# Kernel optimization log

Measured on AMD Instinct MI355X. Metric: run time of the kernel, lower is better.

The kernel has to match this reference:

```python
import jax, jax.numpy as jnp
import numpy as np

E = 1024
H = 16
F = 4096
EPS = 1e-5


def layer_norm(x, gamma, beta):
    mu = jnp.mean(x, axis=-1, keepdims=True)
    var = jnp.var(x, axis=-1, keepdims=True)
    return (x - mu) * jax.lax.rsqrt(var + EPS) * gamma + beta


def setup_inputs() -> dict:
    key = jax.random.key(0)
    ks = jax.random.split(key, 12)
    s = lambda d: 1.0 / np.sqrt(d)
    x = jax.random.normal(ks[0], (2, 2048, E), dtype=jnp.float32)
    Wq = jax.random.uniform(ks[1], (E, E), minval=-s(E), maxval=s(E))
    bq = jnp.zeros((E,), jnp.float32)
    Wk = jax.random.uniform(ks[2], (E, E), minval=-s(E), maxval=s(E))
    bk = jnp.zeros((E,), jnp.float32)
    Wv = jax.random.uniform(ks[3], (E, E), minval=-s(E), maxval=s(E))
    bv = jnp.zeros((E,), jnp.float32)
    Wo = jax.random.uniform(ks[4], (E, E), minval=-s(E), maxval=s(E))
    bo = jnp.zeros((E,), jnp.float32)
    g1 = jnp.ones((E,), jnp.float32)
    b1 = jnp.zeros((E,), jnp.float32)
    W1 = jax.random.uniform(ks[5], (E, F), minval=-s(E), maxval=s(E))
    bf1 = jnp.zeros((F,), jnp.float32)
    W2 = jax.random.uniform(ks[6], (F, E), minval=-s(F), maxval=s(F))
    bf2 = jnp.zeros((E,), jnp.float32)
    g2 = jnp.ones((E,), jnp.float32)
    b2 = jnp.zeros((E,), jnp.float32)
    return dict(x=x, Wq=Wq, bq=bq, Wk=Wk, bk=bk, Wv=Wv, bv=bv, Wo=Wo, bo=bo,
                g1=g1, b1=b1, W1=W1, bf1=bf1, W2=W2, bf2=bf2, g2=g2, b2=b2)


def reference(x, Wq, bq, Wk, bk, Wv, bv, Wo, bo, g1, b1, W1, bf1, W2, bf2, g2, b2):
    B, L, _ = x.shape
    Dh = E // H
    q = (x @ Wq + bq).reshape(B, L, H, Dh).transpose(0, 2, 1, 3)  # b h l d
    k = (x @ Wk + bk).reshape(B, L, H, Dh).transpose(0, 2, 1, 3)  # computed but unused (faithful to source)
    v = (x @ Wv + bv).reshape(B, L, H, Dh).transpose(0, 2, 1, 3)
    # NOTE: source computes scores as Q @ V^T (not K), scaled, then softmax
    scores = jnp.einsum('bhqd,bhkd->bhqk', q, v) / jnp.sqrt(jnp.float32(Dh))
    att = jax.nn.softmax(scores, axis=-1)
    ctx = jnp.einsum('bhqk,bhkd->bhqd', att, v)
    ctx = ctx.transpose(0, 2, 1, 3).reshape(B, L, E)
    att_out = ctx @ Wo + bo
    post_att = layer_norm(x + att_out, g1, b1)
    ff = jax.nn.relu(post_att @ W1 + bf1) @ W2 + bf2
    return layer_norm(post_att + ff, g2, b2)
```

## Files before the change

### kernel.cpp

```cpp
#include <hip/hip_runtime.h>
#include <stdint.h>

typedef unsigned short u16;
typedef __attribute__((ext_vector_type(8))) short short8;
typedef __attribute__((ext_vector_type(4))) float f32x4;
typedef __attribute__((ext_vector_type(4))) unsigned short u16x4;

#define TOKENS 4096
#define E_DIM 1024
#define F_DIM 4096
#define SEQ 2048
#define NH 16
#define DH 64

__device__ __forceinline__ u16 f2b(float f) {
  union { float f; unsigned u; } v; v.f = f;
  unsigned r = v.u + 0x7fffu + ((v.u >> 16) & 1u);
  return (u16)(r >> 16);
}

__device__ __forceinline__ void gl2lds16(const u16* g, u16* l) {
  __builtin_amdgcn_global_load_lds(
      (const __attribute__((address_space(1))) unsigned int*)(size_t)(g),
      (__attribute__((address_space(3))) unsigned int*)(unsigned int)(size_t)(l),
      16, 0, 0);
}


__global__ __launch_bounds__(256)
void transpose_w(const float* __restrict__ W, u16* __restrict__ Wt, int K, int N) {
  __shared__ float tile[32][33];
  const int kb = blockIdx.x * 32, nb = blockIdx.y * 32;
  const int tx = threadIdx.x & 31, ty = threadIdx.x >> 5;
#pragma unroll
  for (int i = 0; i < 32; i += 8)
    tile[ty + i][tx] = W[(size_t)(kb + ty + i) * N + nb + tx];
  __syncthreads();
#pragma unroll
  for (int i = 0; i < 32; i += 8)
    Wt[(size_t)(nb + ty + i) * K + kb + tx] = f2b(tile[tx][ty + i]);
}

__global__ __launch_bounds__(256)
void f32_to_bf16(const float* __restrict__ in, u16* __restrict__ out) {
  const int i = blockIdx.x * 256 + threadIdx.x;
  f32x4 f = ((const f32x4*)in)[i];
  u16x4 u;
#pragma unroll
  for (int j = 0; j < 4; j++) u[j] = f2b(f[j]);
  ((u16x4*)out)[i] = u;
}

__global__ __launch_bounds__(256)
void transpose_v(const u16* __restrict__ vsrc, u16* __restrict__ vt) {
  __shared__ u16 tile[64][66];
  const int kb = blockIdx.x * 64;
  const int bh = blockIdx.y;
  const int b = bh >> 4, h = bh & 15;
  {
    const int d = threadIdx.x & 63, r = threadIdx.x >> 6;
#pragma unroll
    for (int i = 0; i < 64; i += 4)
      tile[r + i][d] = vsrc[(size_t)(b * SEQ + kb + r + i) * E_DIM + h * DH + d];
  }
  __syncthreads();
  {
    const int pos = threadIdx.x & 63;
    const int srck = (pos & 3) * 16 + (pos >> 2);
#pragma unroll
    for (int j = 0; j < 64; j += 4) {
      const int d = (threadIdx.x >> 6) + j;
      vt[(size_t)(bh * DH + d) * SEQ + kb + pos] = tile[srck][d];
    }
  }
}

template <int RELU, int OUTBF>
__global__ __launch_bounds__(512)
void gemm256(const u16* __restrict__ A, const u16* __restrict__ Bt,
             const float* __restrict__ bias, void* __restrict__ Cout,
             int N, int K) {
  __shared__ __align__(16) u16 lds[3][2][8192];
  const int tid = threadIdx.x;
  const int lane = tid & 63, wave = tid >> 6;
  const int wm = wave >> 2, wn = wave & 3;
  const int l15 = lane & 15, g = lane >> 4;

  const int bid = blockIdx.x;
  const int xcd = bid & 7, idx = bid >> 3;
  const int mT = (xcd >> 2) * 8 + (idx >> 2);
  const int nT = (xcd & 3) * 4 + (idx & 3);
  const int mBlk = mT * 256, nBlk = nT * 256;

  const u16* Ab = A + (size_t)mBlk * K;
  const u16* Bb = Bt + (size_t)nBlk * K;

  const int srow = lane >> 2;
  const int scolx = ((lane & 3) ^ ((lane >> 3) & 3)) * 8;
  const u16* sa0 = Ab + (size_t)(wave * 16 + srow) * K + scolx;
  const u16* sa1 = Ab + (size_t)((8 + wave) * 16 + srow) * K + scolx;
  const u16* sb0 = Bb + (size_t)(wave * 16 + srow) * K + scolx;
  const u16* sb1 = Bb + (size_t)((8 + wave) * 16 + srow) * K + scolx;

  const int fo = l15 * 32 + ((g ^ ((l15 >> 1) & 3)) << 3);

  f32x4 acc[8][4] = {};

  const int NT = K >> 5;

#define STAGE_A(buf, t)                                             \
  {                                                                 \
    gl2lds16(sa0 + (size_t)(t) * 32, &lds[buf][0][wave * 512 + lane * 8]);       \
    gl2lds16(sa1 + (size_t)(t) * 32, &lds[buf][0][(8 + wave) * 512 + lane * 8]); \
  }
#define STAGE_B(buf, t)                                             \
  {                                                                 \
    gl2lds16(sb0 + (size_t)(t) * 32, &lds[buf][1][wave * 512 + lane * 8]);       \
    gl2lds16(sb1 + (size_t)(t) * 32, &lds[buf][1][(8 + wave) * 512 + lane * 8]); \
  }

  STAGE_A(0, 0) STAGE_B(0, 0)
  STAGE_A(1, 1) STAGE_B(1, 1)
  asm volatile("s_waitcnt vmcnt(4)" ::: "memory");
  asm volatile("s_barrier" ::: "memory");

  int buf = 0, sbuf = 2;
  for (int t = 0; t < NT; ++t) {
    const u16* As_ = &lds[buf][0][wm * (8 * 512)];
    const u16* Bs_ = &lds[buf][1][wn * (4 * 512)];

    short8 af[4], bfr[4];
#pragma unroll
    for (int i = 0; i < 4; i++)
      af[i] = *(const short8*)(As_ + i * 512 + fo);
#pragma unroll
    for (int i = 0; i < 4; i++)
      bfr[i] = *(const short8*)(Bs_ + i * 512 + fo);
    if (t + 2 < NT) STAGE_A(sbuf, t + 2)
    asm volatile("s_barrier" ::: "memory");
    asm volatile("s_waitcnt lgkmcnt(0)" ::: "memory");
    __builtin_amdgcn_sched_barrier(0);
    __builtin_amdgcn_s_setprio(1);
#pragma unroll
    for (int mg = 0; mg < 4; mg++)
#pragma unroll
      for (int ng = 0; ng < 4; ng++)
        acc[mg][ng] = __builtin_amdgcn_mfma_f32_16x16x32_bf16(af[mg], bfr[ng],
                                                              acc[mg][ng], 0, 0, 0);
    __builtin_amdgcn_s_setprio(0);
    asm volatile("s_barrier" ::: "memory");

#pragma unroll
    for (int i = 0; i < 4; i++)
      af[i] = *(const short8*)(As_ + (4 + i) * 512 + fo);
    if (t + 2 < NT) STAGE_B(sbuf, t + 2)
    asm volatile("s_barrier" ::: "memory");
    asm volatile("s_waitcnt lgkmcnt(0)" ::: "memory");
    __builtin_amdgcn_sched_barrier(0);
    __builtin_amdgcn_s_setprio(1);
#pragma unroll
    for (int mg = 0; mg < 4; mg++)
#pragma unroll
      for (int ng = 0; ng < 4; ng++)
        acc[4 + mg][ng] = __builtin_amdgcn_mfma_f32_16x16x32_bf16(af[mg], bfr[ng],
                                                                  acc[4 + mg][ng], 0, 0, 0);
    __builtin_amdgcn_s_setprio(0);
    if (t + 2 < NT) asm volatile("s_waitcnt vmcnt(4)" ::: "memory");
    else            asm volatile("s_waitcnt vmcnt(0)" ::: "memory");
    asm volatile("s_barrier" ::: "memory");

    buf = (buf == 2) ? 0 : buf + 1;
    sbuf = (sbuf == 2) ? 0 : sbuf + 1;
  }
#undef STAGE_A
#undef STAGE_B

  const int row0 = mBlk + wm * 128 + g * 4;
  const int col0 = nBlk + wn * 64 + l15;
#pragma unroll
  for (int ng = 0; ng < 4; ng++) {
    const int c = col0 + ng * 16;
    const float bv = bias[c];
#pragma unroll
    for (int mg = 0; mg < 8; mg++) {
#pragma unroll
      for (int r = 0; r < 4; r++) {
        float v = acc[mg][ng][r] + bv;
        if (RELU) v = fmaxf(v, 0.f);
        const size_t o = (size_t)(row0 + mg * 16 + r) * N + c;
        if (OUTBF) ((u16*)Cout)[o] = f2b(v);
        else       ((float*)Cout)[o] = v;
      }
    }
  }
}

__global__ __launch_bounds__(512)
void gemm_wide_sk(const u16* __restrict__ A, const u16* __restrict__ Bt,
                  const float* __restrict__ bias, float* __restrict__ Cout,
                  int N, int K) {
  __shared__ __align__(16) u16 lds[3][12288];
  const int tid = threadIdx.x;
  const int lane = tid & 63, wave = tid >> 6;
  const int wm = wave >> 1, wn = wave & 1;
  const int l15 = lane & 15, g = lane >> 4;

  const int bid = blockIdx.x;
  const int xcd = bid & 7, idx = bid >> 3;
  const int kz = xcd & 1;
  const int nT = ((xcd >> 1) & 1) * 4 + (idx & 3);
  const int mT = (xcd >> 2) * 8 + (idx >> 2);
  const int mBlk = mT * 256, nBlk = nT * 128;
  const int Kh = K >> 1;

  const u16* Ab = A + (size_t)mBlk * K + (size_t)kz * Kh;
  const u16* Bb = Bt + (size_t)nBlk * K + (size_t)kz * Kh;

  const int srow = lane >> 2;
  const int scolx = ((lane & 3) ^ ((lane >> 3) & 3)) * 8;
  const u16* sa0 = Ab + (size_t)(wave * 16 + srow) * K + scolx;
  const u16* sa1 = Ab + (size_t)((8 + wave) * 16 + srow) * K + scolx;
  const u16* sb0 = Bb + (size_t)(wave * 16 + srow) * K + scolx;

  const int fo = l15 * 32 + ((g ^ ((l15 >> 1) & 3)) << 3);

  f32x4 acc[4][4] = {};
  const int NT = Kh >> 5;

#define WSTAGE(buf, t)                                                         \
  {                                                                            \
    gl2lds16(sa0 + (size_t)(t) * 32, &lds[buf][wave * 512 + lane * 8]);        \
    gl2lds16(sa1 + (size_t)(t) * 32, &lds[buf][(8 + wave) * 512 + lane * 8]);  \
    gl2lds16(sb0 + (size_t)(t) * 32, &lds[buf][8192 + wave * 512 + lane * 8]); \
  }

  WSTAGE(0, 0)
  WSTAGE(1, 1)
  asm volatile("s_waitcnt vmcnt(3)" ::: "memory");
  asm volatile("s_barrier" ::: "memory");

  int buf = 0, sbuf = 2;
  for (int t = 0; t < NT; ++t) {
    const u16* As_ = &lds[buf][wm * (4 * 512)];
    const u16* Bs_ = &lds[buf][8192 + wn * (4 * 512)];
    short8 af[4], bfr[4];
#pragma unroll
    for (int i = 0; i < 4; i++)
      af[i] = *(const short8*)(As_ + i * 512 + fo);
#pragma unroll
    for (int i = 0; i < 4; i++)
      bfr[i] = *(const short8*)(Bs_ + i * 512 + fo);
    if (t + 2 < NT) WSTAGE(sbuf, t + 2)
    asm volatile("s_waitcnt lgkmcnt(0)" ::: "memory");
    __builtin_amdgcn_sched_barrier(0);
    __builtin_amdgcn_s_setprio(1);
#pragma unroll
    for (int mi = 0; mi < 4; mi++)
#pragma unroll
      for (int ni = 0; ni < 4; ni++)
        acc[mi][ni] = __builtin_amdgcn_mfma_f32_16x16x32_bf16(af[mi], bfr[ni],
                                                              acc[mi][ni], 0, 0, 0);
    __builtin_amdgcn_s_setprio(0);
    if (t + 2 < NT) asm volatile("s_waitcnt vmcnt(3)" ::: "memory");
    else            asm volatile("s_waitcnt vmcnt(0)" ::: "memory");
    asm volatile("s_barrier" ::: "memory");
    buf = (buf == 2) ? 0 : buf + 1;
    sbuf = (sbuf == 2) ? 0 : sbuf + 1;
  }
#undef WSTAGE

  float* out = Cout + (size_t)kz * TOKENS * N;
  const int row0 = mBlk + wm * 64 + g * 4;
  const int col0 = nBlk + wn * 64 + l15;
#pragma unroll
  for (int ni = 0; ni < 4; ni++) {
    const int c = col0 + ni * 16;
    const float bv = (kz == 0) ? bias[c] : 0.f;
#pragma unroll
    for (int mi = 0; mi < 4; mi++) {
#pragma unroll
      for (int r = 0; r < 4; r++)
        out[(size_t)(row0 + mi * 16 + r) * N + c] = acc[mi][ni][r] + bv;
    }
  }
}

__global__ __launch_bounds__(256)
void gemm_qv64(const u16* __restrict__ A, const u16* __restrict__ Bqv,
               const float* __restrict__ bq, const float* __restrict__ bv,
               u16* __restrict__ qout, u16* __restrict__ vout, int K) {
  __shared__ __align__(16) u16 As[128 * 32];
  __shared__ __align__(16) u16 Bs[64 * 32];
  const int tid = threadIdx.x;
  const int lane = tid & 63, wave = tid >> 6;
  const int mBlk = blockIdx.y * 128, nBlk = blockIdx.x * 64;
  const int isQ = nBlk < 1024;
  const int ncol = isQ ? nBlk : nBlk - 1024;
  const float* bias = isQ ? bq : bv;
  u16* out = isQ ? qout : vout;
  const float oscale = isQ ? 0.125f * 1.44269504088896f : 1.0f;
  const int wm = (wave >> 1) * 64, wn = (wave & 1) * 32;
  const int l15 = lane & 15, g = lane >> 4;

  f32x4 acc[4][2] = {};
  const int srow = lane >> 2;
  const int scolx = ((lane & 3) ^ ((lane >> 3) & 3)) * 8;
  const int fo = l15 * 32 + ((g ^ ((l15 >> 1) & 3)) << 3);

  const u16* Ab = A + (size_t)mBlk * K;
  const u16* Bb = Bqv + (size_t)nBlk * K;

  for (int k0 = 0; k0 < K; k0 += 32) {
    __syncthreads();
    for (int c = wave; c < 8; c += 4)
      gl2lds16(Ab + (size_t)(c * 16 + srow) * K + k0 + scolx, As + c * 512 + lane * 8);
    gl2lds16(Bb + (size_t)(wave * 16 + srow) * K + k0 + scolx, Bs + wave * 512 + lane * 8);
    __syncthreads();

    short8 af[4], bf[2];
#pragma unroll
    for (int i = 0; i < 4; i++)
      af[i] = *(const short8*)(As + ((wm >> 4) + i) * 512 + fo);
#pragma unroll
    for (int i = 0; i < 2; i++)
      bf[i] = *(const short8*)(Bs + ((wn >> 4) + i) * 512 + fo);
#pragma unroll
    for (int mi = 0; mi < 4; mi++)
#pragma unroll
      for (int ni = 0; ni < 2; ni++)
        acc[mi][ni] = __builtin_amdgcn_mfma_f32_16x16x32_bf16(af[mi], bf[ni],
                                                              acc[mi][ni], 0, 0, 0);
  }

  const int row0 = mBlk + wm + g * 4;
  const int col0 = ncol + wn + l15;
#pragma unroll
  for (int ni = 0; ni < 2; ni++) {
    const int c = col0 + ni * 16;
    const float bv_ = bias[c];
#pragma unroll
    for (int mi = 0; mi < 4; mi++) {
#pragma unroll
      for (int r = 0; r < 4; r++) {
        float v = (acc[mi][ni][r] + bv_) * oscale;
        out[(size_t)(row0 + mi * 16 + r) * E_DIM + c] = f2b(v);
      }
    }
  }
}

__global__ __launch_bounds__(256)
void attn_kernel(const u16* __restrict__ qb, const u16* __restrict__ vb,
                 const u16* __restrict__ vtb, u16* __restrict__ ctxb) {
  __shared__ __align__(16) u16 Vs[2][4096];
  __shared__ __align__(16) u16 Vts[2][4096];
  __shared__ __align__(16) u16 Pl[4][1024];
  const int tid = threadIdx.x;
  const int lane = tid & 63;
  const int wave = tid >> 6;
  const int l15 = lane & 15;
  const int g = lane >> 4;
  const int l7 = l15 & 7;
  const int qblk = blockIdx.x;
  const int bh = blockIdx.y;
  const int b = bh >> 4;
  const int h = bh & 15;
  const int qrow = qblk * 64 + wave * 16;

  short8 aq0, aq1;
  {
    const u16* qp = qb + ((size_t)(b * SEQ + qrow + l15)) * E_DIM + h * DH + g * 8;
    aq0 = *(const short8*)(qp);
    aq1 = *(const short8*)(qp + 32);
  }

  f32x4 o[4] = {};
  float lsum[4] = {};

  u16* myPl = Pl[wave];

  const u16* qk0b0 = Vs[0] + l15 * 64 + ((g ^ l7) * 8);
  const u16* qk1b0 = Vs[0] + l15 * 64 + (((4 + g) ^ l7) * 8);
  const u16* bv0b0 = Vts[0] + l15 * 64 + ((g ^ l7) * 8);
  const u16* bv1b0 = Vts[0] + l15 * 64 + (((4 + g) ^ l7) * 8);
  const u16* ap0 = myPl + l15 * 64 + ((g ^ l7) << 3);
  const u16* ap1 = myPl + l15 * 64 + (((4 + g) ^ l7) << 3);
  u16* wr0 = myPl + (g * 4 + 0) * 64 + (((l15 >> 1) ^ ((g * 4 + 0) & 7)) << 3) + ((l15 & 1) << 2);
  u16* wr1 = myPl + (g * 4 + 1) * 64 + (((l15 >> 1) ^ ((g * 4 + 1) & 7)) << 3) + ((l15 & 1) << 2);
  u16* wr2 = myPl + (g * 4 + 2) * 64 + (((l15 >> 1) ^ ((g * 4 + 2) & 7)) << 3) + ((l15 & 1) << 2);
  u16* wr3 = myPl + (g * 4 + 3) * 64 + (((l15 >> 1) ^ ((g * 4 + 3) & 7)) << 3) + ((l15 & 1) << 2);

  const int srow = tid >> 3;
  const int sch = tid & 7;
  const int r0 = srow, r1 = 32 + srow;
  const u16* pv0 = vb + ((size_t)(b * SEQ) + r0) * E_DIM + h * DH + ((sch ^ (r0 & 7)) * 8);
  const u16* pv1 = vb + ((size_t)(b * SEQ) + r1) * E_DIM + h * DH + ((sch ^ (r1 & 7)) * 8);
  const u16* pt0 = vtb + ((size_t)bh * DH + r0) * SEQ + ((sch ^ (r0 & 7)) * 8);
  const u16* pt1 = vtb + ((size_t)bh * DH + r1) * SEQ + ((sch ^ (r1 & 7)) * 8);

#define STAGE(buf)                                      \
  {                                                     \
    gl2lds16(pv0, Vs[buf] + tid * 8);                   \
    gl2lds16(pv1, Vs[buf] + 2048 + tid * 8);            \
    gl2lds16(pt0, Vts[buf] + tid * 8);                  \
    gl2lds16(pt1, Vts[buf] + 2048 + tid * 8);           \
    pv0 += 64 * E_DIM; pv1 += 64 * E_DIM;               \
    pt0 += 64; pt1 += 64;                               \
  }

#define SMROW(r, WR)                                                          \
  {                                                                           \
    union { float f; unsigned u; } p0, p1, p2, p3;                            \
    p0.f = __builtin_amdgcn_exp2f(s[0][r]);                                   \
    p1.f = __builtin_amdgcn_exp2f(s[1][r]);                                   \
    p2.f = __builtin_amdgcn_exp2f(s[2][r]);                                   \
    p3.f = __builtin_amdgcn_exp2f(s[3][r]);                                   \
    union { unsigned u; float f; } t0, t1, t2, t3;                            \
    t0.u = p0.u & 0xffff0000u; t1.u = p1.u & 0xffff0000u;                     \
    t2.u = p2.u & 0xffff0000u; t3.u = p3.u & 0xffff0000u;                     \
    lsum[r] += (t0.f + t1.f) + (t2.f + t3.f);                                 \
    uint2 pk;                                                                 \
    pk.x = __builtin_amdgcn_perm(p1.u, p0.u, 0x07060302u);                    \
    pk.y = __builtin_amdgcn_perm(p3.u, p2.u, 0x07060302u);                    \
    *(uint2*)(WR) = pk;                                                       \
  }

#define COMPUTE(QK0, QK1, BV0, BV1)                                           \
  {                                                                           \
    f32x4 s[4];                                                               \
    _Pragma("unroll") for (int nt = 0; nt < 4; nt++) {                        \
      short8 b0 = *(const short8*)((QK0) + nt * 1024);                        \
      short8 b1 = *(const short8*)((QK1) + nt * 1024);                        \
      f32x4 z = {};                                                           \
      z = __builtin_amdgcn_mfma_f32_16x16x32_bf16(aq0, b0, z, 0, 0, 0);       \
      z = __builtin_amdgcn_mfma_f32_16x16x32_bf16(aq1, b1, z, 0, 0, 0);       \
      s[nt] = z;                                                              \
    }                                                                         \
    SMROW(0, wr0) SMROW(1, wr1) SMROW(2, wr2) SMROW(3, wr3)                   \
    {                                                                         \
      short8 ap = *(const short8*)ap0;                                        \
      _Pragma("unroll") for (int dt = 0; dt < 4; dt++) {                      \
        short8 bvv = *(const short8*)((BV0) + dt * 1024);                     \
        o[dt] = __builtin_amdgcn_mfma_f32_16x16x32_bf16(ap, bvv, o[dt], 0, 0, 0); \
      }                                                                       \
      ap = *(const short8*)ap1;                                               \
      _Pragma("unroll") for (int dt = 0; dt < 4; dt++) {                      \
        short8 bvv = *(const short8*)((BV1) + dt * 1024);                     \
        o[dt] = __builtin_amdgcn_mfma_f32_16x16x32_bf16(ap, bvv, o[dt], 0, 0, 0); \
      }                                                                       \
    }                                                                         \
  }

#define HALF(CB, EN)                                                          \
  {                                                                           \
    asm volatile("s_barrier" ::: "memory");                                   \
    if (EN) {                                                                 \
      STAGE(CB ^ 1)                                                           \
      asm volatile("s_waitcnt vmcnt(4)" ::: "memory");                        \
    } else {                                                                  \
      asm volatile("s_waitcnt vmcnt(0)" ::: "memory");                        \
    }                                                                         \
    asm volatile("s_barrier" ::: "memory");                                   \
    if (CB == 0) { COMPUTE(qk0b0, qk1b0, bv0b0, bv1b0) }                      \
    else { COMPUTE(qk0b0 + 4096, qk1b0 + 4096, bv0b0 + 4096, bv1b0 + 4096) }  \
  }

  STAGE(0)
#pragma unroll 1
  for (int it = 0; it < 15; ++it) {
    HALF(0, 1)
    HALF(1, 1)
  }
  HALF(0, 1)
  HALF(1, 0)

#undef HALF
#undef COMPUTE
#undef SMROW
#undef STAGE

#pragma unroll
  for (int r = 0; r < 4; r++) {
    float l = lsum[r];
    l += __shfl_xor(l, 1);
    l += __shfl_xor(l, 2);
    l += __shfl_xor(l, 4);
    l += __shfl_xor(l, 8);
    const float inv = 1.0f / l;
    size_t base = ((size_t)(b * SEQ + qrow + g * 4 + r)) * E_DIM + h * DH;
#pragma unroll
    for (int dt = 0; dt < 4; dt++)
      ctxb[base + dt * 16 + l15] = f2b(o[dt][r] * inv);
  }
}

__global__ __launch_bounds__(256)
void add_ln3(const float* __restrict__ X, const float* __restrict__ Y0,
             const float* __restrict__ Y1,
             const float* __restrict__ gam, const float* __restrict__ bet,
             float* __restrict__ out32, u16* __restrict__ out16) {
  const int row = blockIdx.x;
  const int tid = threadIdx.x;
  const size_t base = (size_t)row * E_DIM;
  float v[4];
  float s = 0.f, sq = 0.f;
#pragma unroll
  for (int i = 0; i < 4; i++) {
    const int c = tid + i * 256;
    float x = X[base + c] + Y0[base + c] + Y1[base + c];
    v[i] = x; s += x; sq += x * x;
  }
#pragma unroll
  for (int off = 32; off; off >>= 1) {
    s += __shfl_xor(s, off);
    sq += __shfl_xor(sq, off);
  }
  __shared__ float sh[8];
  const int wave = tid >> 6, lane = tid & 63;
  if (lane == 0) { sh[wave] = s; sh[4 + wave] = sq; }
  __syncthreads();
  s = sh[0] + sh[1] + sh[2] + sh[3];
  sq = sh[4] + sh[5] + sh[6] + sh[7];
  const float mean = s * (1.f / 1024.f);
  const float var = sq * (1.f / 1024.f) - mean * mean;
  const float rstd = rsqrtf(var + 1e-5f);
#pragma unroll
  for (int i = 0; i < 4; i++) {
    const int c = tid + i * 256;
    float y = (v[i] - mean) * rstd * gam[c] + bet[c];
    out32[base + c] = y;
    if (out16) out16[base + c] = f2b(y);
  }
}

extern "C" void kernel_launch(void* const* d_in, const int* in_sizes, int n_in,
                              void* d_out, int out_size, void* d_ws, size_t ws_size,
                              hipStream_t stream) {
  const float* x   = (const float*)d_in[0];
  const float* Wq  = (const float*)d_in[1];
  const float* bq  = (const float*)d_in[2];
  const float* Wv  = (const float*)d_in[5];
  const float* bv  = (const float*)d_in[6];
  const float* Wo  = (const float*)d_in[7];
  const float* bo  = (const float*)d_in[8];
  const float* g1  = (const float*)d_in[9];
  const float* b1  = (const float*)d_in[10];
  const float* W1  = (const float*)d_in[11];
  const float* bf1 = (const float*)d_in[12];
  const float* W2  = (const float*)d_in[13];
  const float* bf2 = (const float*)d_in[14];
  const float* g2  = (const float*)d_in[15];
  const float* b2  = (const float*)d_in[16];

  char* w = (char*)d_ws;
  const size_t MB = 1024ull * 1024ull;
  u16*   xb   = (u16*)(w + 0);
  u16*   h1   = (u16*)(w + 8 * MB);
  u16*   qb   = (u16*)(w + 8 * MB);
  u16*   vb   = (u16*)(w + 16 * MB);
  u16*   vtb  = (u16*)(w + 24 * MB);
  u16*   ctxb = (u16*)(w + 32 * MB);
  float* att0 = (float*)(w + 40 * MB);
  float* ff0  = (float*)(w + 40 * MB);
  float* pa   = (float*)(w + 72 * MB);
  u16*   pab  = (u16*)(w + 88 * MB);
  u16*   WqT  = (u16*)(w + 96 * MB);
  u16*   WvT  = (u16*)(w + 98 * MB);
  u16*   WoT  = (u16*)(w + 100 * MB);
  u16*   W1T  = (u16*)(w + 102 * MB);
  u16*   W2T  = (u16*)(w + 110 * MB);

  transpose_w<<<dim3(32, 32), 256, 0, stream>>>(Wq, WqT, 1024, 1024);
  transpose_w<<<dim3(32, 32), 256, 0, stream>>>(Wv, WvT, 1024, 1024);
  transpose_w<<<dim3(32, 32), 256, 0, stream>>>(Wo, WoT, 1024, 1024);
  transpose_w<<<dim3(32, 128), 256, 0, stream>>>(W1, W1T, 1024, 4096);
  transpose_w<<<dim3(128, 32), 256, 0, stream>>>(W2, W2T, 4096, 1024);
  f32_to_bf16<<<TOKENS * E_DIM / 4 / 256, 256, 0, stream>>>(x, xb);

  gemm_qv64<<<dim3(32, 32), 256, 0, stream>>>(xb, WqT, bq, bv, qb, vb, 1024);
  transpose_v<<<dim3(32, 32), 256, 0, stream>>>(vb, vtb);
  attn_kernel<<<dim3(32, 32), 256, 0, stream>>>(qb, vb, vtb, ctxb);
  gemm_wide_sk<<<dim3(256), 512, 0, stream>>>(ctxb, WoT, bo, att0, 1024, 1024);
  add_ln3<<<TOKENS, 256, 0, stream>>>(x, att0, att0 + (size_t)TOKENS * 1024, g1, b1, pa, pab);
  gemm256<1, 1><<<dim3(256), 512, 0, stream>>>(pab, W1T, bf1, h1, 4096, 1024);
  gemm_wide_sk<<<dim3(256), 512, 0, stream>>>(h1, W2T, bf2, ff0, 1024, 4096);
  add_ln3<<<TOKENS, 256, 0, stream>>>(pa, ff0, ff0 + (size_t)TOKENS * 1024, g2, b2, (float*)d_out, (u16*)nullptr);
}
```

Baseline: 352.1 us.

## Pre-swizzle V^T into MFMA fragment order and load B operands straight to registers

The V-transpose kernel now writes V^T already arranged in per-lane MFMA B-fragment order, 64-key chunk by chunk. The attention kernel then loads those fragments directly from global memory into registers with vector loads, dropping the Vts LDS buffer and its LDS reads. The vmcnt waits are retuned to cover the extra outstanding loads. The 2D grid is flattened and remapped so that blocks sharing a batch-head land on the same XCD, to improve L2 reuse of V. In exchange it uses more vector registers and relies on more global loads being in flight.

New measurement: 356.5 us. No clear change (+1.3%).

```diff
diff --git a/kernel.cpp b/kernel.cpp
--- a/kernel.cpp
+++ b/kernel.cpp
@@ -64,15 +64,24 @@
       tile[r + i][d] = vsrc[(size_t)(b * SEQ + kb + r + i) * E_DIM + h * DH + d];
   }
   __syncthreads();
-  {
-    const int pos = threadIdx.x & 63;
-    const int srck = (pos & 3) * 16 + (pos >> 2);
-#pragma unroll
-    for (int j = 0; j < 64; j += 4) {
-      const int d = (threadIdx.x >> 6) + j;
-      vt[(size_t)(bh * DH + d) * SEQ + kb + pos] = tile[srck][d];
-    }
-  }
+  u16* outb = vt + (size_t)bh * (SEQ * DH) + (size_t)(kb >> 6) * 4096;
+  const int idx0 = threadIdx.x * 16;
+  union { u16 v[16]; uint4 q[2]; } u;
+#pragma unroll
+  for (int w = 0; w < 16; w++) {
+    const int idx = idx0 + w;
+    const int frag = idx >> 9;
+    const int lane2 = (idx >> 3) & 63;
+    const int j = idx & 7;
+    const int ks = frag >> 2, dt = frag & 3;
+    const int g2 = lane2 >> 4, lf = lane2 & 15;
+    const int d = dt * 16 + lf;
+    const int pos = (ks * 4 + g2) * 8 + j;
+    const int key = (pos & 3) * 16 + (pos >> 2);
+    u.v[w] = tile[key][d];
+  }
+  *(uint4*)(outb + idx0) = u.q[0];
+  *(uint4*)(outb + idx0 + 8) = u.q[1];
 }
 
 template <int RELU, int OUTBF>
@@ -353,7 +362,6 @@
 void attn_kernel(const u16* __restrict__ qb, const u16* __restrict__ vb,
                  const u16* __restrict__ vtb, u16* __restrict__ ctxb) {
   __shared__ __align__(16) u16 Vs[2][4096];
-  __shared__ __align__(16) u16 Vts[2][4096];
   __shared__ __align__(16) u16 Pl[4][1024];
   const int tid = threadIdx.x;
   const int lane = tid & 63;
@@ -361,8 +369,9 @@
   const int l15 = lane & 15;
   const int g = lane >> 4;
   const int l7 = l15 & 7;
-  const int qblk = blockIdx.x;
-  const int bh = blockIdx.y;
+  const int bid = blockIdx.x;
+  const int bh = (bid & 7) * 4 + ((bid >> 3) & 3);
+  const int qblk = bid >> 5;
   const int b = bh >> 4;
   const int h = bh & 15;
   const int qrow = qblk * 64 + wave * 16;
@@ -376,13 +385,12 @@
 
   f32x4 o[4] = {};
   float lsum[4] = {};
+  short8 bvr[8];
 
   u16* myPl = Pl[wave];
 
   const u16* qk0b0 = Vs[0] + l15 * 64 + ((g ^ l7) * 8);
   const u16* qk1b0 = Vs[0] + l15 * 64 + (((4 + g) ^ l7) * 8);
-  const u16* bv0b0 = Vts[0] + l15 * 64 + ((g ^ l7) * 8);
-  const u16* bv1b0 = Vts[0] + l15 * 64 + (((4 + g) ^ l7) * 8);
   const u16* ap0 = myPl + l15 * 64 + ((g ^ l7) << 3);
   const u16* ap1 = myPl + l15 * 64 + (((4 + g) ^ l7) << 3);
   u16* wr0 = myPl + (g * 4 + 0) * 64 + (((l15 >> 1) ^ ((g * 4 + 0) & 7)) << 3) + ((l15 & 1) << 2);
@@ -395,17 +403,21 @@
   const int r0 = srow, r1 = 32 + srow;
   const u16* pv0 = vb + ((size_t)(b * SEQ) + r0) * E_DIM + h * DH + ((sch ^ (r0 & 7)) * 8);
   const u16* pv1 = vb + ((size_t)(b * SEQ) + r1) * E_DIM + h * DH + ((sch ^ (r1 & 7)) * 8);
-  const u16* pt0 = vtb + ((size_t)bh * DH + r0) * SEQ + ((sch ^ (r0 & 7)) * 8);
-  const u16* pt1 = vtb + ((size_t)bh * DH + r1) * SEQ + ((sch ^ (r1 & 7)) * 8);
+
+  const u16* bvp = vtb + (size_t)bh * (SEQ * DH) + lane * 8;
 
 #define STAGE(buf)                                      \
   {                                                     \
     gl2lds16(pv0, Vs[buf] + tid * 8);                   \
     gl2lds16(pv1, Vs[buf] + 2048 + tid * 8);            \
-    gl2lds16(pt0, Vts[buf] + tid * 8);                  \
-    gl2lds16(pt1, Vts[buf] + 2048 + tid * 8);           \
     pv0 += 64 * E_DIM; pv1 += 64 * E_DIM;               \
-    pt0 += 64; pt1 += 64;                               \
+  }
+
+#define BVLOAD()                                        \
+  {                                                     \
+    _Pragma("unroll") for (int f = 0; f < 8; f++)       \
+      bvr[f] = *(const short8*)(bvp + f * 512);         \
+    bvp += 4096;                                        \
   }
 
 #define SMROW(r, WR)                                                          \
@@ -425,7 +437,7 @@
     *(uint2*)(WR) = pk;                                                       \
   }
 
-#define COMPUTE(QK0, QK1, BV0, BV1)                                           \
+#define COMPUTE(QK0, QK1, VMB)                                                \
   {                                                                           \
     f32x4 s[4];                                                               \
     _Pragma("unroll") for (int nt = 0; nt < 4; nt++) {                        \
@@ -437,46 +449,45 @@
       s[nt] = z;                                                              \
     }                                                                         \
     SMROW(0, wr0) SMROW(1, wr1) SMROW(2, wr2) SMROW(3, wr3)                   \
+    asm volatile(VMB ::: "memory");                                           \
     {                                                                         \
       short8 ap = *(const short8*)ap0;                                        \
-      _Pragma("unroll") for (int dt = 0; dt < 4; dt++) {                      \
-        short8 bvv = *(const short8*)((BV0) + dt * 1024);                     \
-        o[dt] = __builtin_amdgcn_mfma_f32_16x16x32_bf16(ap, bvv, o[dt], 0, 0, 0); \
-      }                                                                       \
+      o[0] = __builtin_amdgcn_mfma_f32_16x16x32_bf16(ap, bvr[0], o[0], 0, 0, 0); \
+      o[1] = __builtin_amdgcn_mfma_f32_16x16x32_bf16(ap, bvr[1], o[1], 0, 0, 0); \
+      o[2] = __builtin_amdgcn_mfma_f32_16x16x32_bf16(ap, bvr[2], o[2], 0, 0, 0); \
+      o[3] = __builtin_amdgcn_mfma_f32_16x16x32_bf16(ap, bvr[3], o[3], 0, 0, 0); \
       ap = *(const short8*)ap1;                                               \
-      _Pragma("unroll") for (int dt = 0; dt < 4; dt++) {                      \
-        short8 bvv = *(const short8*)((BV1) + dt * 1024);                     \
-        o[dt] = __builtin_amdgcn_mfma_f32_16x16x32_bf16(ap, bvv, o[dt], 0, 0, 0); \
-      }                                                                       \
+      o[0] = __builtin_amdgcn_mfma_f32_16x16x32_bf16(ap, bvr[4], o[0], 0, 0, 0); \
+      o[1] = __builtin_amdgcn_mfma_f32_16x16x32_bf16(ap, bvr[5], o[1], 0, 0, 0); \
+      o[2] = __builtin_amdgcn_mfma_f32_16x16x32_bf16(ap, bvr[6], o[2], 0, 0, 0); \
+      o[3] = __builtin_amdgcn_mfma_f32_16x16x32_bf16(ap, bvr[7], o[3], 0, 0, 0); \
     }                                                                         \
   }
 
-#define HALF(CB, EN)                                                          \
+#define HALF(CB, EN, VMA, VMB)                                                \
   {                                                                           \
     asm volatile("s_barrier" ::: "memory");                                   \
-    if (EN) {                                                                 \
-      STAGE(CB ^ 1)                                                           \
-      asm volatile("s_waitcnt vmcnt(4)" ::: "memory");                        \
-    } else {                                                                  \
-      asm volatile("s_waitcnt vmcnt(0)" ::: "memory");                        \
-    }                                                                         \
+    BVLOAD()                                                                  \
+    if (EN) { STAGE(CB ^ 1) }                                                 \
+    asm volatile(VMA ::: "memory");                                           \
     asm volatile("s_barrier" ::: "memory");                                   \
-    if (CB == 0) { COMPUTE(qk0b0, qk1b0, bv0b0, bv1b0) }                      \
-    else { COMPUTE(qk0b0 + 4096, qk1b0 + 4096, bv0b0 + 4096, bv1b0 + 4096) }  \
+    if (CB == 0) { COMPUTE(qk0b0, qk1b0, VMB) }                               \
+    else { COMPUTE(qk0b0 + 4096, qk1b0 + 4096, VMB) }                         \
   }
 
   STAGE(0)
 #pragma unroll 1
   for (int it = 0; it < 15; ++it) {
-    HALF(0, 1)
-    HALF(1, 1)
-  }
-  HALF(0, 1)
-  HALF(1, 0)
+    HALF(0, 1, "s_waitcnt vmcnt(10)", "s_waitcnt vmcnt(2)")
+    HALF(1, 1, "s_waitcnt vmcnt(10)", "s_waitcnt vmcnt(2)")
+  }
+  HALF(0, 1, "s_waitcnt vmcnt(10)", "s_waitcnt vmcnt(2)")
+  HALF(1, 0, "s_waitcnt vmcnt(8)", "s_waitcnt vmcnt(0)")
 
 #undef HALF
 #undef COMPUTE
 #undef SMROW
+#undef BVLOAD
 #undef STAGE
 
 #pragma unroll
@@ -579,7 +590,7 @@
 
   gemm_qv64<<<dim3(32, 32), 256, 0, stream>>>(xb, WqT, bq, bv, qb, vb, 1024);
   transpose_v<<<dim3(32, 32), 256, 0, stream>>>(vb, vtb);
-  attn_kernel<<<dim3(32, 32), 256, 0, stream>>>(qb, vb, vtb, ctxb);
+  attn_kernel<<<dim3(1024), 256, 0, stream>>>(qb, vb, vtb, ctxb);
   gemm_wide_sk<<<dim3(256), 512, 0, stream>>>(ctxb, WoT, bo, att0, 1024, 1024);
   add_ln3<<<TOKENS, 256, 0, stream>>>(x, att0, att0 + (size_t)TOKENS * 1024, g1, b1, pa, pab);
   gemm256<1, 1><<<dim3(256), 512, 0, stream>>>(pab, W1T, bf1, h1, 4096, 1024);
```

## Triple-buffer Q/V projection GEMM loads and vectorize add+layernorm

Applied to the files above, without the earlier changes.

The Q/V projection GEMM now uses a three-stage LDS ring buffer, prefetching two K-tiles ahead with async global-to-LDS loads. Each iteration waits with explicit vmcnt/lgkmcnt counts instead of two __syncthreads, and raises wave priority around the MFMA block, so memory latency overlaps with compute. Separately, the add+layernorm kernel switches to 128-bit vector loads and stores, with each thread owning four contiguous columns. In exchange the GEMM uses more LDS, which may lower occupancy, and correctness now depends on the hand-written wait counts.

Measured after the change: 359.2 us. 1.02x slower.

```diff
diff --git a/kernel.cpp b/kernel.cpp
--- a/kernel.cpp
+++ b/kernel.cpp
@@ -289,8 +289,7 @@
 void gemm_qv64(const u16* __restrict__ A, const u16* __restrict__ Bqv,
                const float* __restrict__ bq, const float* __restrict__ bv,
                u16* __restrict__ qout, u16* __restrict__ vout, int K) {
-  __shared__ __align__(16) u16 As[128 * 32];
-  __shared__ __align__(16) u16 Bs[64 * 32];
+  __shared__ __align__(16) u16 lds[3][6144];
   const int tid = threadIdx.x;
   const int lane = tid & 63, wave = tid >> 6;
   const int mBlk = blockIdx.y * 128, nBlk = blockIdx.x * 64;
@@ -309,28 +308,53 @@
 
   const u16* Ab = A + (size_t)mBlk * K;
   const u16* Bb = Bqv + (size_t)nBlk * K;
-
-  for (int k0 = 0; k0 < K; k0 += 32) {
-    __syncthreads();
-    for (int c = wave; c < 8; c += 4)
-      gl2lds16(Ab + (size_t)(c * 16 + srow) * K + k0 + scolx, As + c * 512 + lane * 8);
-    gl2lds16(Bb + (size_t)(wave * 16 + srow) * K + k0 + scolx, Bs + wave * 512 + lane * 8);
-    __syncthreads();
-
-    short8 af[4], bf[2];
+  const u16* sa0 = Ab + (size_t)(wave * 16 + srow) * K + scolx;
+  const u16* sa1 = Ab + (size_t)((4 + wave) * 16 + srow) * K + scolx;
+  const u16* sb0 = Bb + (size_t)(wave * 16 + srow) * K + scolx;
+
+  const int NT = K >> 5;
+
+#define QSTAGE(buf, t)                                                         \
+  {                                                                            \
+    gl2lds16(sa0 + (size_t)(t) * 32, &lds[buf][wave * 512 + lane * 8]);        \
+    gl2lds16(sa1 + (size_t)(t) * 32, &lds[buf][(4 + wave) * 512 + lane * 8]);  \
+    gl2lds16(sb0 + (size_t)(t) * 32, &lds[buf][4096 + wave * 512 + lane * 8]); \
+  }
+
+  QSTAGE(0, 0)
+  QSTAGE(1, 1)
+  asm volatile("s_waitcnt vmcnt(3)" ::: "memory");
+  asm volatile("s_barrier" ::: "memory");
+
+  int buf = 0, sbuf = 2;
+  for (int t = 0; t < NT; ++t) {
+    const u16* As_ = &lds[buf][(wave >> 1) * (4 * 512)];
+    const u16* Bs_ = &lds[buf][4096 + (wave & 1) * (2 * 512)];
+    short8 af[4], bfr[2];
 #pragma unroll
     for (int i = 0; i < 4; i++)
-      af[i] = *(const short8*)(As + ((wm >> 4) + i) * 512 + fo);
+      af[i] = *(const short8*)(As_ + i * 512 + fo);
 #pragma unroll
     for (int i = 0; i < 2; i++)
-      bf[i] = *(const short8*)(Bs + ((wn >> 4) + i) * 512 + fo);
+      bfr[i] = *(const short8*)(Bs_ + i * 512 + fo);
+    if (t + 2 < NT) QSTAGE(sbuf, t + 2)
+    asm volatile("s_waitcnt lgkmcnt(0)" ::: "memory");
+    __builtin_amdgcn_sched_barrier(0);
+    __builtin_amdgcn_s_setprio(1);
 #pragma unroll
     for (int mi = 0; mi < 4; mi++)
 #pragma unroll
       for (int ni = 0; ni < 2; ni++)
-        acc[mi][ni] = __builtin_amdgcn_mfma_f32_16x16x32_bf16(af[mi], bf[ni],
+        acc[mi][ni] = __builtin_amdgcn_mfma_f32_16x16x32_bf16(af[mi], bfr[ni],
                                                               acc[mi][ni], 0, 0, 0);
-  }
+    __builtin_amdgcn_s_setprio(0);
+    if (t + 2 < NT) asm volatile("s_waitcnt vmcnt(3)" ::: "memory");
+    else            asm volatile("s_waitcnt vmcnt(0)" ::: "memory");
+    asm volatile("s_barrier" ::: "memory");
+    buf = (buf == 2) ? 0 : buf + 1;
+    sbuf = (sbuf == 2) ? 0 : sbuf + 1;
+  }
+#undef QSTAGE
 
   const int row0 = mBlk + wm + g * 4;
   const int col0 = ncol + wn + l15;
@@ -502,13 +526,16 @@
   const int row = blockIdx.x;
   const int tid = threadIdx.x;
   const size_t base = (size_t)row * E_DIM;
-  float v[4];
+  const int c4 = tid * 4;
+  f32x4 x = *(const f32x4*)(X + base + c4);
+  f32x4 y0 = *(const f32x4*)(Y0 + base + c4);
+  f32x4 y1 = *(const f32x4*)(Y1 + base + c4);
+  f32x4 v;
   float s = 0.f, sq = 0.f;
 #pragma unroll
   for (int i = 0; i < 4; i++) {
-    const int c = tid + i * 256;
-    float x = X[base + c] + Y0[base + c] + Y1[base + c];
-    v[i] = x; s += x; sq += x * x;
+    float t = x[i] + y0[i] + y1[i];
+    v[i] = t; s += t; sq += t * t;
   }
 #pragma unroll
   for (int off = 32; off; off >>= 1) {
@@ -524,13 +551,17 @@
   const float mean = s * (1.f / 1024.f);
   const float var = sq * (1.f / 1024.f) - mean * mean;
   const float rstd = rsqrtf(var + 1e-5f);
+  f32x4 gm = *(const f32x4*)(gam + c4);
+  f32x4 bt = *(const f32x4*)(bet + c4);
+  f32x4 y;
+  u16x4 yb;
 #pragma unroll
   for (int i = 0; i < 4; i++) {
-    const int c = tid + i * 256;
-    float y = (v[i] - mean) * rstd * gam[c] + bet[c];
-    out32[base + c] = y;
-    if (out16) out16[base + c] = f2b(y);
-  }
+    y[i] = (v[i] - mean) * rstd * gm[i] + bt[i];
+    yb[i] = f2b(y[i]);
+  }
+  *(f32x4*)(out32 + base + c4) = y;
+  if (out16) *(u16x4*)(out16 + base + c4) = yb;
 }
 
 extern "C" void kernel_launch(void* const* d_in, const int* in_sizes, int n_in,
```
